# Performance work log

Measured on AMD Instinct MI355X. Metric: run time of the kernel, lower is better.

The kernel has to match this reference:

```python
import jax, jax.numpy as jnp
import numpy as np

B, T, C, H, W = 4, 5, 512, 32, 32   # bt = B*T = 20
G = 32                              # GroupNorm groups
EPS = 1e-6


def group_norm(x, gamma, beta):
    # x: [N, C, H, W]; normalize per (group-channels, H, W)
    n, c, h, w = x.shape
    xg = x.reshape(n, G, c // G, h * w)
    mu = jnp.mean(xg, axis=(2, 3), keepdims=True)
    var = jnp.mean((xg - mu) ** 2, axis=(2, 3), keepdims=True)
    xn = ((xg - mu) * jax.lax.rsqrt(var + EPS)).reshape(n, c, h, w)
    return xn * gamma[None, :, None, None] + beta[None, :, None, None]


def conv1x1(x, w, b):
    # 1x1 conv == channel matmul. x: [N,C,H,W], w: [O,C], b: [O]
    return jnp.einsum('nchw,oc->nohw', x, w) + b[None, :, None, None]


def setup_inputs() -> dict:
    key = jax.random.key(0)
    ks = jax.random.split(key, 9)
    inp = {'x': jax.random.normal(ks[0], (B * T, C, H, W), jnp.float32)}
    for i, nm in enumerate(['wq', 'wk', 'wv', 'wo', 'wqt', 'wkt', 'wvt', 'wot']):
        inp[nm] = jax.random.normal(ks[i + 1], (C, C), jnp.float32) * 0.02
        inp['b' + nm[1:]] = jnp.zeros((C,), jnp.float32)
    inp['gamma_s'] = jnp.ones((C,), jnp.float32)
    inp['beta_s'] = jnp.zeros((C,), jnp.float32)
    inp['gamma_t'] = jnp.ones((C,), jnp.float32)
    inp['beta_t'] = jnp.zeros((C,), jnp.float32)
    return inp


def reference(x, wq, bq, wk, bk, wv, bv, wo, bo,
              wqt, bqt, wkt, bkt, wvt, bvt, wot, bot,
              gamma_s, beta_s, gamma_t, beta_t):
    scale = float(C) ** -0.5

    # ---- spatial attention (AttnBlock.forward) ----
    hn = group_norm(x, gamma_s, beta_s)
    q = conv1x1(hn, wq, bq).reshape(B * T, C, H * W)
    k = conv1x1(hn, wk, bk).reshape(B * T, C, H * W)
    v = conv1x1(hn, wv, bv).reshape(B * T, C, H * W)
    # scores [bt, hw_q, hw_k], softmax over keys
    att = jax.nn.softmax(jnp.einsum('bcq,bck->bqk', q, k) * scale, axis=2)
    hsp = jnp.einsum('bck,bqk->bcq', v, att).reshape(B * T, C, H, W)
    spatio = x + conv1x1(hsp, wo, bo)

    # ---- temporal attention across t=5 frames per pixel ----
    hn = group_norm(spatio, gamma_t, beta_t)
    q5 = conv1x1(hn, wqt, bqt).reshape(B, T, C, H, W)
    k5 = conv1x1(hn, wkt, bkt).reshape(B, T, C, H, W)
    v5 = conv1x1(hn, wvt, bvt).reshape(B, T, C, H, W)
    # per-pixel [t, t] attention, softmax over key-frame axis s
    att_t = jax.nn.softmax(jnp.einsum('btchw,bschw->bhwts', q5, k5) * scale, axis=-1)
    htp = jnp.einsum('bhwts,bschw->btchw', att_t, v5).reshape(B * T, C, H, W)

    # NOTE: residual is the ORIGINAL x (faithful to the source), not spatio
    return x + conv1x1(htp, wot, bot)
```

## Files before the change

kernel.cpp:

```cpp
#include <hip/hip_runtime.h>
#include <hip/hip_bf16.h>
#include <stdint.h>

typedef unsigned short u16;
typedef __attribute__((ext_vector_type(8))) short bf16x8;
typedef __attribute__((ext_vector_type(4))) float f32x4;

#define DI __device__ __forceinline__

DI float b2f(u16 u) { return __uint_as_float(((uint32_t)u) << 16); }
DI u16 f2b(float f) {
  uint32_t u = __float_as_uint(f);
  u += 0x7fff + ((u >> 16) & 1);
  return (u16)(u >> 16);
}

DI void gld_lds16(const u16* g, u16* l) {
  __builtin_amdgcn_global_load_lds((const __attribute__((address_space(1))) void*)g,
                                   (__attribute__((address_space(3))) void*)l,
                                   16, 0, 0);
}

__global__ __launch_bounds__(256)
void prep(const float* __restrict__ x, const float* __restrict__ gamma,
          const float* __restrict__ beta, u16* __restrict__ gnout,
          const float* __restrict__ w0, const float* __restrict__ w1,
          const float* __restrict__ w2, const float* __restrict__ w3,
          const float* __restrict__ w4, const float* __restrict__ w5,
          const float* __restrict__ w6, const float* __restrict__ w7,
          const float* __restrict__ b0, const float* __restrict__ b1,
          const float* __restrict__ b2, const float* __restrict__ b3,
          const float* __restrict__ b4, const float* __restrict__ b5,
          const float* __restrict__ b6, const float* __restrict__ b7,
          u16* __restrict__ dst, float* __restrict__ bdst)
{
  const int t = threadIdx.x;
  if (blockIdx.x < 640) {
    const int w = (blockIdx.x & 7) * 80 + (blockIdx.x >> 3);
    const int n = w >> 5, g = w & 31;
    const int C = 512, HW = 1024;
    const float* xg = x + ((long)n * C + g * 16) * HW;
    float s = 0.f, ss = 0.f;
    for (int ch = t; ch < 4096; ch += 256) {
      float4 u = *(const float4*)(xg + ch * 4);
      s += u.x + u.y + u.z + u.w;
      ss += u.x * u.x + u.y * u.y + u.z * u.z + u.w * u.w;
    }
#pragma unroll
    for (int off = 32; off > 0; off >>= 1) { s += __shfl_xor(s, off); ss += __shfl_xor(ss, off); }
    __shared__ float rs[4], rss[4];
    if ((t & 63) == 0) { rs[t >> 6] = s; rss[t >> 6] = ss; }
    __syncthreads();
    s  = rs[0] + rs[1] + rs[2] + rs[3];
    ss = rss[0] + rss[1] + rss[2] + rss[3];
    const float mu = s * (1.f / 16384.f);
    const float var = ss * (1.f / 16384.f) - mu * mu;
    const float rstd = rsqrtf(var + 1e-6f);
    float gm[16], bt[16];
#pragma unroll
    for (int i = 0; i < 16; ++i) {
      float ga = gamma[g * 16 + i];
      gm[i] = ga * rstd;
      bt[i] = beta[g * 16 + i] - mu * ga * rstd;
    }
    for (int p = t; p < 1024; p += 256) {
      alignas(16) u16 vals[16];
#pragma unroll
      for (int i = 0; i < 16; ++i)
        vals[i] = f2b(xg[(long)i * HW + p] * gm[i] + bt[i]);
      u16* dp = gnout + ((long)n * HW + p) * C + g * 16;
      *(uint4*)dp       = *(const uint4*)&vals[0];
      *(uint4*)(dp + 8) = *(const uint4*)&vals[8];
    }
    return;
  }
  const int sb = blockIdx.x - 640;
  if (sb >= 1034) {
    bdst[8192 + (sb - 1034) * 256 + t] = 0.f;
    return;
  }
  if (sb >= 1032) {
    const int a = (sb - 1032) * 256 + t;
    float acc = 0.f;
    for (int c = 0; c < 512; ++c) acc += w3[a * 512 + c] * b2[c];
    bdst[4096 + a] = acc;
    return;
  }
  if (sb >= 1024) {
    const float* bs8[8] = {b0, b1, b2, b3, b4, b5, b6, b7};
    const int a = sb - 1024;
    bdst[a * 512 + t] = bs8[a][t];
    bdst[a * 512 + t + 256] = bs8[a][t + 256];
    return;
  }
  const float* srcs[8] = {w0, w1, w2, w3, w4, w5, w6, w7};
  const int mat = sb >> 7;
  const int i = (((sb & 127) << 8) + t) * 8;
  const float* s = srcs[mat];
  float4 a = *(const float4*)(s + i);
  float4 b = *(const float4*)(s + i + 4);
  alignas(16) u16 v[8] = {f2b(a.x), f2b(a.y), f2b(a.z), f2b(a.w),
                          f2b(b.x), f2b(b.y), f2b(b.z), f2b(b.w)};
  *(uint4*)(dst + (long)mat * 262144 + i) = *(const uint4*)v;
  if (mat == 2) {
    const int row = i >> 9, col = i & 511;
#pragma unroll
    for (int j = 0; j < 8; ++j) dst[8 * 262144 + (col + j) * 512 + row] = v[j];
  }
}

template<int OUTF32, int BIASMODE, int RESID, int SMEXP, int COLSCALE>
__global__ __launch_bounds__(256)
void gemm_bt(const u16* __restrict__ A, long sA, long lda,
             const u16* __restrict__ B, long sB, long ldb,
             void* __restrict__ C, long sC,
             const float* __restrict__ bias,
             const float* __restrict__ resid, long sR,
             int N, int K, float alpha, float* __restrict__ stats)
{
  __shared__ u16 lA[2 * 128 * 32];
  __shared__ u16 lB[2 * 128 * 32];
  const int t = threadIdx.x;
  const int lane = t & 63;
  const int wid = t >> 6;

  const uint32_t nx = gridDim.x, ny = gridDim.y;
  const uint32_t tpz = nx * ny;
  const uint32_t nblk = tpz * gridDim.z;
  const uint32_t g = ((uint32_t)blockIdx.z * ny + blockIdx.y) * nx + blockIdx.x;
  const uint32_t idx = (g & 7u) * (nblk >> 3) + (g >> 3);
  const uint32_t bz_ = idx / tpz;
  const uint32_t r   = idx - bz_ * tpz;
  const int m0 = (int)(r / nx) * 128, n0 = (int)(r % nx) * 128;
  const long bz = bz_;

  const u16* Ab = A + bz * sA;
  const u16* Bb = B + bz * sB;

  const int row = t >> 2;
  const int kc  = (((t & 3) ^ ((t >> 3) & 3)) << 3);

  f32x4 acc[4][4];
#pragma unroll
  for (int i = 0; i < 4; ++i)
#pragma unroll
    for (int j = 0; j < 4; ++j) acc[i][j] = (f32x4){0.f, 0.f, 0.f, 0.f};

  const int ml = lane & 15, qd = lane >> 4;
  const int koff = ((qd ^ ((ml >> 1) & 3)) << 3);
  const int wm = (wid >> 1) * 64, wn = (wid & 1) * 64;

  auto stage = [&](int bsel, int k0) {
    const u16* Ap = Ab + (long)(m0 + row) * lda + (k0 + kc);
    const u16* Bp = Bb + (long)(n0 + row) * ldb + (k0 + kc);
    u16* la = lA + bsel * 4096 + wid * 512;
    u16* lb = lB + bsel * 4096 + wid * 512;
    gld_lds16(Ap, la);
    gld_lds16(Ap + 64 * lda, la + 2048);
    gld_lds16(Bp, lb);
    gld_lds16(Bp + 64 * ldb, lb + 2048);
  };

  const int niter = K >> 5;
  stage(0, 0);
  for (int i = 0; i < niter; ++i) {
    __syncthreads();
    if (i + 1 < niter) stage((i + 1) & 1, (i + 1) << 5);
    const u16* la = lA + (i & 1) * 4096;
    const u16* lb = lB + (i & 1) * 4096;
    bf16x8 af[4], bfr[4];
#pragma unroll
    for (int x = 0; x < 4; ++x)
      af[x] = *(const bf16x8*)&la[(wm + x * 16 + ml) * 32 + koff];
#pragma unroll
    for (int y = 0; y < 4; ++y)
      bfr[y] = *(const bf16x8*)&lb[(wn + y * 16 + ml) * 32 + koff];
#pragma unroll
    for (int x = 0; x < 4; ++x)
#pragma unroll
      for (int y = 0; y < 4; ++y)
        acc[x][y] = __builtin_amdgcn_mfma_f32_16x16x32_bf16(af[x], bfr[y], acc[x][y], 0, 0, 0);
  }

  float inv[4];
  if (COLSCALE) {
#pragma unroll
    for (int j = 0; j < 4; ++j)
      inv[j] = 1.f / stats[bz * 1024 + n0 + wn + j * 16 + ml];
  }
  if (SMEXP) {
    float rs[16];
#pragma unroll
    for (int s = 0; s < 16; ++s) rs[s] = 0.f;
#pragma unroll
    for (int i = 0; i < 4; ++i)
#pragma unroll
      for (int j = 0; j < 4; ++j)
#pragma unroll
        for (int r2 = 0; r2 < 4; ++r2) {
          float e = __expf(acc[i][j][r2] * alpha);
          acc[i][j][r2] = e;
          rs[i * 4 + r2] += e;
        }
#pragma unroll
    for (int m = 1; m < 16; m <<= 1)
#pragma unroll
      for (int s = 0; s < 16; ++s) rs[s] += __shfl_xor(rs[s], m);
    if (ml == 0) {
#pragma unroll
      for (int i = 0; i < 4; ++i)
#pragma unroll
        for (int r2 = 0; r2 < 4; ++r2)
          atomicAdd(&stats[bz * 1024 + m0 + wm + i * 16 + qd * 4 + r2], rs[i * 4 + r2]);
    }
  }

  const long cb = bz * sC;
#pragma unroll
  for (int i = 0; i < 4; ++i) {
#pragma unroll
    for (int j = 0; j < 4; ++j) {
#pragma unroll
      for (int r2 = 0; r2 < 4; ++r2) {
        int rr = m0 + wm + i * 16 + qd * 4 + r2;
        int cc = n0 + wn + j * 16 + ml;
        float v = acc[i][j][r2];
        if (!SMEXP) v *= alpha;
        if (COLSCALE) v *= inv[j];
        if (BIASMODE == 1) v += bias[rr];
        if (BIASMODE == 2) v += bias[cc];
        long ix = (long)rr * N + cc;
        if (RESID) v += resid[bz * sR + ix];
        if (OUTF32) ((float*)C)[cb + ix] = v;
        else        ((u16*)C)[cb + ix] = f2b(v);
      }
    }
  }
}

template<int OUTF32, int BIASMODE, int RESID>
__global__ __launch_bounds__(512, 2)
void gemm256(const u16* __restrict__ A, long sA, long lda,
             const u16* __restrict__ B, long sB, long ldb,
             void* __restrict__ C, long sC,
             const float* __restrict__ bias,
             const float* __restrict__ resid, long sR,
             int N, int K, float alpha)
{
  __shared__ u16 lA[4 * 8192];
  __shared__ u16 lB[4 * 8192];
  const int t = threadIdx.x;
  const int lane = t & 63, wid = t >> 6;
  const int wr = wid >> 2, wc = wid & 3;
  const int ml = lane & 15, qd = lane >> 4;

  const int nx = gridDim.x;
  const int bid = blockIdx.y * nx + blockIdx.x;
  const int nper = (nx * gridDim.y) >> 3;
  const int nid = (bid & 7) * nper + (bid >> 3);
  const int m0 = (nid / nx) * 256, n0 = (nid % nx) * 256;

  const long bz = blockIdx.z;
  const u16* Ab = A + bz * sA;
  const u16* Bb = B + bz * sB;

  const int sw = ((lane & 3) ^ ((lane >> 3) & 3)) << 3;
  const int srow = wid * 32 + (lane >> 2);
  const u16* ApS = Ab + (long)(m0 + srow) * lda + sw;
  const u16* BpS = Bb + (long)(n0 + srow) * ldb + sw;
  u16* lwA = lA + wid * 1024;
  u16* lwB = lB + wid * 1024;

  f32x4 acc[8][4];
#pragma unroll
  for (int i = 0; i < 8; ++i)
#pragma unroll
    for (int j = 0; j < 4; ++j) acc[i][j] = (f32x4){0.f, 0.f, 0.f, 0.f};

  const int NT = K >> 5;

  auto stageA = [&](int tk) {
    const int bo = (tk & 3) << 13;
    const u16* p = ApS + ((long)tk << 5);
    gld_lds16(p,              lwA + bo);
    gld_lds16(p + (lda << 4), lwA + bo + 512);
  };
  auto stageB = [&](int tk) {
    const int bo = (tk & 3) << 13;
    const u16* p = BpS + ((long)tk << 5);
    gld_lds16(p,              lwB + bo);
    gld_lds16(p + (ldb << 4), lwB + bo + 512);
  };

  const int koff = (qd ^ ((ml >> 1) & 3)) << 3;
  const int rAo = (wr * 128 + ml) * 32 + koff;
  const int rBo = (wc * 64 + ml) * 32 + koff;

  stageA(0); stageB(0); stageA(1); stageB(1); stageA(2); stageB(2);
  asm volatile("s_waitcnt vmcnt(8)" ::: "memory");
  __builtin_amdgcn_s_barrier();
  __builtin_amdgcn_sched_barrier(0);

  for (int tk = 0; tk < NT; ++tk) {
    const int bo = (tk & 3) << 13;
    const u16* pa = lA + bo + rAo;
    const u16* pb = lB + bo + rBo;
    bf16x8 bfr[4], af[4];

#pragma unroll
    for (int n = 0; n < 4; ++n) bfr[n] = *(const bf16x8*)(pb + n * 512);
#pragma unroll
    for (int m = 0; m < 4; ++m) af[m] = *(const bf16x8*)(pa + m * 512);
    if (tk + 3 < NT) stageA(tk + 3);
    __builtin_amdgcn_sched_barrier(0);
    __builtin_amdgcn_s_barrier();
    asm volatile("s_waitcnt lgkmcnt(0)" ::: "memory");
    __builtin_amdgcn_sched_barrier(0);
    __builtin_amdgcn_s_setprio(1);
#pragma unroll
    for (int m = 0; m < 4; ++m)
#pragma unroll
      for (int n = 0; n < 4; ++n)
        acc[m][n] = __builtin_amdgcn_mfma_f32_16x16x32_bf16(af[m], bfr[n], acc[m][n], 0, 0, 0);
    __builtin_amdgcn_s_setprio(0);
    __builtin_amdgcn_sched_barrier(0);
    __builtin_amdgcn_s_barrier();
    __builtin_amdgcn_sched_barrier(0);

#pragma unroll
    for (int m = 0; m < 4; ++m) af[m] = *(const bf16x8*)(pa + (m + 4) * 512);
    if (tk + 3 < NT) stageB(tk + 3);
    __builtin_amdgcn_sched_barrier(0);
    __builtin_amdgcn_s_barrier();
    asm volatile("s_waitcnt lgkmcnt(0)" ::: "memory");
    __builtin_amdgcn_sched_barrier(0);
    __builtin_amdgcn_s_setprio(1);
#pragma unroll
    for (int m = 0; m < 4; ++m)
#pragma unroll
      for (int n = 0; n < 4; ++n)
        acc[m + 4][n] = __builtin_amdgcn_mfma_f32_16x16x32_bf16(af[m], bfr[n], acc[m + 4][n], 0, 0, 0);
    __builtin_amdgcn_s_setprio(0);
    __builtin_amdgcn_sched_barrier(0);

    if (tk < NT - 1) {
      const int rem = NT - 2 - tk;
      if (rem >= 2)      asm volatile("s_waitcnt vmcnt(8)" ::: "memory");
      else if (rem == 1) asm volatile("s_waitcnt vmcnt(4)" ::: "memory");
      else               asm volatile("s_waitcnt vmcnt(0)" ::: "memory");
      __builtin_amdgcn_s_barrier();
      __builtin_amdgcn_sched_barrier(0);
    }
  }

  const long cb = bz * sC;
#pragma unroll
  for (int mt = 0; mt < 8; ++mt) {
#pragma unroll
    for (int nt = 0; nt < 4; ++nt) {
#pragma unroll
      for (int r = 0; r < 4; ++r) {
        int rr = m0 + wr * 128 + mt * 16 + qd * 4 + r;
        int cc = n0 + wc * 64 + nt * 16 + ml;
        float v = acc[mt][nt][r] * alpha;
        if (BIASMODE == 1) v += bias[rr];
        if (BIASMODE == 2) v += bias[cc];
        long idx = (long)rr * N + cc;
        if (RESID) v += resid[bz * sR + idx];
        if (OUTF32) ((float*)C)[cb + idx] = v;
        else        ((u16*)C)[cb + idx] = f2b(v);
      }
    }
  }
}

__global__ __launch_bounds__(256)
void groupnorm_resid(const u16* __restrict__ h, const float* __restrict__ x,
                     const float* __restrict__ gamma,
                     const float* __restrict__ beta, u16* __restrict__ out)
{
  const int C = 512, HW = 1024;
  const int w = (blockIdx.x & 7) * 80 + (blockIdx.x >> 3);
  const int n = w >> 5, g = w & 31;
  const long base = ((long)n * C + g * 16) * HW;
  const float* xg = x + base;
  const u16*  hg = h + base;
  const int t = threadIdx.x;
  float s = 0.f, ss = 0.f;
  for (int ch = t; ch < 4096; ch += 256) {
    float4 u = *(const float4*)(xg + ch * 4);
    uint2 hv = *(const uint2*)(hg + ch * 4);
    float h0 = __uint_as_float(hv.x << 16);
    float h1 = __uint_as_float(hv.x & 0xffff0000u);
    float h2 = __uint_as_float(hv.y << 16);
    float h3 = __uint_as_float(hv.y & 0xffff0000u);
    float v0 = u.x + h0, v1 = u.y + h1, v2 = u.z + h2, v3 = u.w + h3;
    s += v0 + v1 + v2 + v3;
    ss += v0 * v0 + v1 * v1 + v2 * v2 + v3 * v3;
  }
#pragma unroll
  for (int off = 32; off > 0; off >>= 1) { s += __shfl_xor(s, off); ss += __shfl_xor(ss, off); }
  __shared__ float rs[4], rss[4];
  if ((t & 63) == 0) { rs[t >> 6] = s; rss[t >> 6] = ss; }
  __syncthreads();
  s  = rs[0] + rs[1] + rs[2] + rs[3];
  ss = rss[0] + rss[1] + rss[2] + rss[3];
  const float mu = s * (1.f / 16384.f);
  const float var = ss * (1.f / 16384.f) - mu * mu;
  const float rstd = rsqrtf(var + 1e-6f);
  float gm[16], bt[16];
#pragma unroll
  for (int i = 0; i < 16; ++i) {
    float ga = gamma[g * 16 + i];
    gm[i] = ga * rstd;
    bt[i] = beta[g * 16 + i] - mu * ga * rstd;
  }
  for (int p = t; p < 1024; p += 256) {
    alignas(16) u16 vals[16];
#pragma unroll
    for (int i = 0; i < 16; ++i)
      vals[i] = f2b((xg[(long)i * HW + p] + b2f(hg[(long)i * HW + p])) * gm[i] + bt[i]);
    u16* dst = out + ((long)n * HW + p) * C + g * 16;
    *(uint4*)dst       = *(const uint4*)&vals[0];
    *(uint4*)(dst + 8) = *(const uint4*)&vals[8];
  }
}

__global__ __launch_bounds__(256)
void temporal_attn(const u16* __restrict__ qkv, u16* __restrict__ htp)
{
  const int t = threadIdx.x;
  const int wv = t >> 6, lane = t & 63;
  const int pix = blockIdx.x * 4 + wv;
  const int b = pix >> 10, p = pix & 1023;
  const long fs = 1024l * 1536;
  const long rowbase = ((long)b * 5 * 1024 + p) * 1536 + lane * 8;

  float qf[5][8], kf[5][8];
#pragma unroll
  for (int f = 0; f < 5; ++f) {
    bf16x8 qv = *(const bf16x8*)(qkv + rowbase + f * fs);
    bf16x8 kv = *(const bf16x8*)(qkv + rowbase + f * fs + 512);
#pragma unroll
    for (int u = 0; u < 8; ++u) { qf[f][u] = b2f((u16)qv[u]); kf[f][u] = b2f((u16)kv[u]); }
  }
  float sc[25];
#pragma unroll
  for (int i = 0; i < 5; ++i)
#pragma unroll
    for (int j = 0; j < 5; ++j) {
      float a = 0.f;
#pragma unroll
      for (int u = 0; u < 8; ++u) a += qf[i][u] * kf[j][u];
      sc[i * 5 + j] = a;
    }
#pragma unroll
  for (int m = 1; m < 64; m <<= 1)
#pragma unroll
    for (int s = 0; s < 25; ++s) sc[s] += __shfl_xor(sc[s], m);

  const float scale = 0.04419417382415922f;
  float att[5][5];
#pragma unroll
  for (int i = 0; i < 5; ++i) {
    float m = sc[i * 5];
#pragma unroll
    for (int j = 1; j < 5; ++j) m = fmaxf(m, sc[i * 5 + j]);
    float ssum = 0.f;
#pragma unroll
    for (int j = 0; j < 5; ++j) { att[i][j] = __expf((sc[i * 5 + j] - m) * scale); ssum += att[i][j]; }
    float inv = 1.f / ssum;
#pragma unroll
    for (int j = 0; j < 5; ++j) att[i][j] *= inv;
  }

  float of[5][8];
#pragma unroll
  for (int i = 0; i < 5; ++i)
#pragma unroll
    for (int u = 0; u < 8; ++u) of[i][u] = 0.f;
#pragma unroll
  for (int s = 0; s < 5; ++s) {
    bf16x8 vvv = *(const bf16x8*)(qkv + rowbase + s * fs + 1024);
#pragma unroll
    for (int u = 0; u < 8; ++u) {
      float vf = b2f((u16)vvv[u]);
#pragma unroll
      for (int i = 0; i < 5; ++i) of[i][u] += att[i][s] * vf;
    }
  }
  const long obase = ((long)b * 5 * 1024 + p) * 512 + lane * 8;
#pragma unroll
  for (int i = 0; i < 5; ++i) {
    alignas(16) u16 ob[8];
#pragma unroll
    for (int u = 0; u < 8; ++u) ob[u] = f2b(of[i][u]);
    *(uint4*)(htp + obase + i * 1024 * 512) = *(const uint4*)ob;
  }
}

extern "C" void kernel_launch(void* const* d_in, const int* in_sizes, int n_in,
                              void* d_out, int out_size, void* d_ws, size_t ws_size,
                              hipStream_t stream)
{
  const float* x   = (const float*)d_in[0];
  const float* wq  = (const float*)d_in[1];
  const float* bq  = (const float*)d_in[2];
  const float* wk  = (const float*)d_in[3];
  const float* bk  = (const float*)d_in[4];
  const float* wv  = (const float*)d_in[5];
  const float* bv  = (const float*)d_in[6];
  const float* wo  = (const float*)d_in[7];
  const float* bo  = (const float*)d_in[8];
  const float* wqt = (const float*)d_in[9];
  const float* bqt = (const float*)d_in[10];
  const float* wkt = (const float*)d_in[11];
  const float* bkt = (const float*)d_in[12];
  const float* wvt = (const float*)d_in[13];
  const float* bvt = (const float*)d_in[14];
  const float* wot = (const float*)d_in[15];
  const float* bot = (const float*)d_in[16];
  const float* gs  = (const float*)d_in[17];
  const float* bs  = (const float*)d_in[18];
  const float* gt  = (const float*)d_in[19];
  const float* btt = (const float*)d_in[20];

  const long U = 20l * 1024 * 512;
  u16* W0 = (u16*)d_ws;
  u16* W1 = W0 + U;
  u16* W3 = W0 + 3 * U;
  u16* W4 = W0 + 4 * U;
  u16* W6 = W0 + 6 * U;
  u16* W7 = W0 + 7 * U;
  u16* Wt = W0 + 8 * U;
  u16* wvT_b = Wt + 8 * 262144;
  u16* Wovs  = Wt + 9 * 262144;
  float* Bf = (float*)(Wt + 10 * 262144);
  float* Stats = Bf + 8192;
  u16* wo_b  = Wt + 3 * 262144;
  u16* wqt_b = Wt + 4 * 262144;
  u16* wot_b = Wt + 7 * 262144;

  const long S  = 524288;
  const long S2 = 1048576;
  const float scale = 0.04419417382415922f;
  dim3 blk(256);
  dim3 blk5(512);

  prep<<<1754, blk, 0, stream>>>(x, gs, bs, W0,
                                 wq, wk, wv, wo, wqt, wkt, wvt, wot,
                                 bq, bk, bv, bo, bqt, bkt, bvt, bot, Wt, Bf);

  gemm_bt<0, 0, 0, 0, 0><<<dim3(4, 4, 1), blk, 0, stream>>>(
      wo_b, 0, 512, wvT_b, 0, 512, Wovs, 0, nullptr, nullptr, 0, 512, 512, 1.f, nullptr);

  gemm_bt<0, 2, 0, 0, 0><<<dim3(8, 160, 1), blk, 0, stream>>>(
      W0, 0, 512, Wt, 0, 512, W1, 0, Bf, nullptr, 0, 1024, 512, 1.f, nullptr);
  gemm_bt<0, 1, 0, 0, 0><<<dim3(8, 4, 20), blk, 0, stream>>>(
      Wovs, 0, 512, W0, S, 512, W3, S, Bf + 4096, nullptr, 0, 1024, 512, 1.f, nullptr);
  gemm_bt<0, 0, 0, 1, 0><<<dim3(8, 8, 20), blk, 0, stream>>>(
      W1, S2, 1024, W1 + 512, S2, 1024, W4, S2, nullptr, nullptr, 0, 1024, 512, scale, Stats);
  gemm_bt<0, 1, 0, 0, 1><<<dim3(8, 4, 20), blk, 0, stream>>>(
      W3, S, 1024, W4, S2, 1024, W6, S, Bf + 1536, nullptr, 0, 1024, 1024, 1.f, Stats);
  groupnorm_resid<<<640, blk, 0, stream>>>(W6, x, gt, btt, W7);
  gemm256<0, 2, 0><<<dim3(6, 80, 1), blk5, 0, stream>>>(
      W7, 0, 512, wqt_b, 0, 512, W1, 0, Bf + 2048, nullptr, 0, 1536, 512, 1.f);
  temporal_attn<<<1024, blk, 0, stream>>>(W1, W0);
  gemm_bt<1, 1, 1, 0, 0><<<dim3(8, 4, 20), blk, 0, stream>>>(
      wot_b, 0, 512, W0, S, 512, (float*)d_out, S, Bf + 3584, x, S, 1024, 512, 1.f, nullptr);
}
```

Baseline: 401.7 us.

## Fold temporal V projection into output projection weights

Computes Wot·Wvt as a combined matrix, using the same trick already applied to the spatial path. The temporal attention therefore reads the normalized input directly as V, and the QKV GEMM shrinks from 1536 to 1024 output columns. The folded bias Wot·bvt + bot is computed in prep, and the custom 256-tile gemm256 kernel is dropped in favor of gemm_bt. This removes one third of the temporal projection FLOPs and the V write/read, at the cost of an extra small 512x512 weight GEMM and losing the larger-tile kernel.

```diff
diff --git a/kernel.cpp b/kernel.cpp
--- a/kernel.cpp
+++ b/kernel.cpp
@@ -75,8 +75,15 @@
     return;
   }
   const int sb = blockIdx.x - 640;
+  if (sb >= 1036) {
+    bdst[8192 + (sb - 1036) * 256 + t] = 0.f;
+    return;
+  }
   if (sb >= 1034) {
-    bdst[8192 + (sb - 1034) * 256 + t] = 0.f;
+    const int a = (sb - 1034) * 256 + t;
+    float acc = 0.f;
+    for (int c = 0; c < 512; ++c) acc += w7[a * 512 + c] * b6[c];
+    bdst[4608 + a] = acc + b7[a];
     return;
   }
   if (sb >= 1032) {
@@ -102,10 +109,11 @@
   alignas(16) u16 v[8] = {f2b(a.x), f2b(a.y), f2b(a.z), f2b(a.w),
                           f2b(b.x), f2b(b.y), f2b(b.z), f2b(b.w)};
   *(uint4*)(dst + (long)mat * 262144 + i) = *(const uint4*)v;
-  if (mat == 2) {
+  if (mat == 2 || mat == 6) {
+    const int slot = (mat == 2) ? 8 : 10;
     const int row = i >> 9, col = i & 511;
 #pragma unroll
-    for (int j = 0; j < 8; ++j) dst[8 * 262144 + (col + j) * 512 + row] = v[j];
+    for (int j = 0; j < 8; ++j) dst[(long)slot * 262144 + (col + j) * 512 + row] = v[j];
   }
 }
 
@@ -233,142 +241,6 @@
         if (RESID) v += resid[bz * sR + ix];
         if (OUTF32) ((float*)C)[cb + ix] = v;
         else        ((u16*)C)[cb + ix] = f2b(v);
-      }
-    }
-  }
-}
-
-template<int OUTF32, int BIASMODE, int RESID>
-__global__ __launch_bounds__(512, 2)
-void gemm256(const u16* __restrict__ A, long sA, long lda,
-             const u16* __restrict__ B, long sB, long ldb,
-             void* __restrict__ C, long sC,
-             const float* __restrict__ bias,
-             const float* __restrict__ resid, long sR,
-             int N, int K, float alpha)
-{
-  __shared__ u16 lA[4 * 8192];
-  __shared__ u16 lB[4 * 8192];
-  const int t = threadIdx.x;
-  const int lane = t & 63, wid = t >> 6;
-  const int wr = wid >> 2, wc = wid & 3;
-  const int ml = lane & 15, qd = lane >> 4;
-
-  const int nx = gridDim.x;
-  const int bid = blockIdx.y * nx + blockIdx.x;
-  const int nper = (nx * gridDim.y) >> 3;
-  const int nid = (bid & 7) * nper + (bid >> 3);
-  const int m0 = (nid / nx) * 256, n0 = (nid % nx) * 256;
-
-  const long bz = blockIdx.z;
-  const u16* Ab = A + bz * sA;
-  const u16* Bb = B + bz * sB;
-
-  const int sw = ((lane & 3) ^ ((lane >> 3) & 3)) << 3;
-  const int srow = wid * 32 + (lane >> 2);
-  const u16* ApS = Ab + (long)(m0 + srow) * lda + sw;
-  const u16* BpS = Bb + (long)(n0 + srow) * ldb + sw;
-  u16* lwA = lA + wid * 1024;
-  u16* lwB = lB + wid * 1024;
-
-  f32x4 acc[8][4];
-#pragma unroll
-  for (int i = 0; i < 8; ++i)
-#pragma unroll
-    for (int j = 0; j < 4; ++j) acc[i][j] = (f32x4){0.f, 0.f, 0.f, 0.f};
-
-  const int NT = K >> 5;
-
-  auto stageA = [&](int tk) {
-    const int bo = (tk & 3) << 13;
-    const u16* p = ApS + ((long)tk << 5);
-    gld_lds16(p,              lwA + bo);
-    gld_lds16(p + (lda << 4), lwA + bo + 512);
-  };
-  auto stageB = [&](int tk) {
-    const int bo = (tk & 3) << 13;
-    const u16* p = BpS + ((long)tk << 5);
-    gld_lds16(p,              lwB + bo);
-    gld_lds16(p + (ldb << 4), lwB + bo + 512);
-  };
-
-  const int koff = (qd ^ ((ml >> 1) & 3)) << 3;
-  const int rAo = (wr * 128 + ml) * 32 + koff;
-  const int rBo = (wc * 64 + ml) * 32 + koff;
-
-  stageA(0); stageB(0); stageA(1); stageB(1); stageA(2); stageB(2);
-  asm volatile("s_waitcnt vmcnt(8)" ::: "memory");
-  __builtin_amdgcn_s_barrier();
-  __builtin_amdgcn_sched_barrier(0);
-
-  for (int tk = 0; tk < NT; ++tk) {
-    const int bo = (tk & 3) << 13;
-    const u16* pa = lA + bo + rAo;
-    const u16* pb = lB + bo + rBo;
-    bf16x8 bfr[4], af[4];
-
-#pragma unroll
-    for (int n = 0; n < 4; ++n) bfr[n] = *(const bf16x8*)(pb + n * 512);
-#pragma unroll
-    for (int m = 0; m < 4; ++m) af[m] = *(const bf16x8*)(pa + m * 512);
-    if (tk + 3 < NT) stageA(tk + 3);
-    __builtin_amdgcn_sched_barrier(0);
-    __builtin_amdgcn_s_barrier();
-    asm volatile("s_waitcnt lgkmcnt(0)" ::: "memory");
-    __builtin_amdgcn_sched_barrier(0);
-    __builtin_amdgcn_s_setprio(1);
-#pragma unroll
-    for (int m = 0; m < 4; ++m)
-#pragma unroll
-      for (int n = 0; n < 4; ++n)
-        acc[m][n] = __builtin_amdgcn_mfma_f32_16x16x32_bf16(af[m], bfr[n], acc[m][n], 0, 0, 0);
-    __builtin_amdgcn_s_setprio(0);
-    __builtin_amdgcn_sched_barrier(0);
-    __builtin_amdgcn_s_barrier();
-    __builtin_amdgcn_sched_barrier(0);
-
-#pragma unroll
-    for (int m = 0; m < 4; ++m) af[m] = *(const bf16x8*)(pa + (m + 4) * 512);
-    if (tk + 3 < NT) stageB(tk + 3);
-    __builtin_amdgcn_sched_barrier(0);
-    __builtin_amdgcn_s_barrier();
-    asm volatile("s_waitcnt lgkmcnt(0)" ::: "memory");
-    __builtin_amdgcn_sched_barrier(0);
-    __builtin_amdgcn_s_setprio(1);
-#pragma unroll
-    for (int m = 0; m < 4; ++m)
-#pragma unroll
-      for (int n = 0; n < 4; ++n)
-        acc[m + 4][n] = __builtin_amdgcn_mfma_f32_16x16x32_bf16(af[m], bfr[n], acc[m + 4][n], 0, 0, 0);
-    __builtin_amdgcn_s_setprio(0);
-    __builtin_amdgcn_sched_barrier(0);
-
-    if (tk < NT - 1) {
-      const int rem = NT - 2 - tk;
-      if (rem >= 2)      asm volatile("s_waitcnt vmcnt(8)" ::: "memory");
-      else if (rem == 1) asm volatile("s_waitcnt vmcnt(4)" ::: "memory");
-      else               asm volatile("s_waitcnt vmcnt(0)" ::: "memory");
-      __builtin_amdgcn_s_barrier();
-      __builtin_amdgcn_sched_barrier(0);
-    }
-  }
-
-  const long cb = bz * sC;
-#pragma unroll
-  for (int mt = 0; mt < 8; ++mt) {
-#pragma unroll
-    for (int nt = 0; nt < 4; ++nt) {
-#pragma unroll
-      for (int r = 0; r < 4; ++r) {
-        int rr = m0 + wr * 128 + mt * 16 + qd * 4 + r;
-        int cc = n0 + wc * 64 + nt * 16 + ml;
-        float v = acc[mt][nt][r] * alpha;
-        if (BIASMODE == 1) v += bias[rr];
-        if (BIASMODE == 2) v += bias[cc];
-        long idx = (long)rr * N + cc;
-        if (RESID) v += resid[bz * sR + idx];
-        if (OUTF32) ((float*)C)[cb + idx] = v;
-        else        ((u16*)C)[cb + idx] = f2b(v);
       }
     }
   }
@@ -427,20 +299,23 @@
 }
 
 __global__ __launch_bounds__(256)
-void temporal_attn(const u16* __restrict__ qkv, u16* __restrict__ htp)
+void temporal_attn(const u16* __restrict__ qk, const u16* __restrict__ hn,
+                   u16* __restrict__ htp)
 {
   const int t = threadIdx.x;
   const int wv = t >> 6, lane = t & 63;
   const int pix = blockIdx.x * 4 + wv;
   const int b = pix >> 10, p = pix & 1023;
-  const long fs = 1024l * 1536;
-  const long rowbase = ((long)b * 5 * 1024 + p) * 1536 + lane * 8;
+  const long fsq = 1024l * 1024;
+  const long rowq = ((long)b * 5 * 1024 + p) * 1024 + lane * 8;
+  const long fsh = 1024l * 512;
+  const long rowh = ((long)b * 5 * 1024 + p) * 512 + lane * 8;
 
   float qf[5][8], kf[5][8];
 #pragma unroll
   for (int f = 0; f < 5; ++f) {
-    bf16x8 qv = *(const bf16x8*)(qkv + rowbase + f * fs);
-    bf16x8 kv = *(const bf16x8*)(qkv + rowbase + f * fs + 512);
+    bf16x8 qv = *(const bf16x8*)(qk + rowq + f * fsq);
+    bf16x8 kv = *(const bf16x8*)(qk + rowq + f * fsq + 512);
 #pragma unroll
     for (int u = 0; u < 8; ++u) { qf[f][u] = b2f((u16)qv[u]); kf[f][u] = b2f((u16)kv[u]); }
   }
@@ -481,7 +356,7 @@
     for (int u = 0; u < 8; ++u) of[i][u] = 0.f;
 #pragma unroll
   for (int s = 0; s < 5; ++s) {
-    bf16x8 vvv = *(const bf16x8*)(qkv + rowbase + s * fs + 1024);
+    bf16x8 vvv = *(const bf16x8*)(hn + rowh + s * fsh);
 #pragma unroll
     for (int u = 0; u < 8; ++u) {
       float vf = b2f((u16)vvv[u]);
@@ -489,13 +364,12 @@
       for (int i = 0; i < 5; ++i) of[i][u] += att[i][s] * vf;
     }
   }
-  const long obase = ((long)b * 5 * 1024 + p) * 512 + lane * 8;
 #pragma unroll
   for (int i = 0; i < 5; ++i) {
     alignas(16) u16 ob[8];
 #pragma unroll
     for (int u = 0; u < 8; ++u) ob[u] = f2b(of[i][u]);
-    *(uint4*)(htp + obase + i * 1024 * 512) = *(const uint4*)ob;
+    *(uint4*)(htp + rowh + i * fsh) = *(const uint4*)ob;
   }
 }
 
@@ -533,39 +407,39 @@
   u16* W6 = W0 + 6 * U;
   u16* W7 = W0 + 7 * U;
   u16* Wt = W0 + 8 * U;
-  u16* wvT_b = Wt + 8 * 262144;
-  u16* Wovs  = Wt + 9 * 262144;
-  float* Bf = (float*)(Wt + 10 * 262144);
+  u16* wvT_b  = Wt + 8 * 262144;
+  u16* Wovs   = Wt + 9 * 262144;
+  u16* Wovt_b = Wt + 11 * 262144;
+  float* Bf = (float*)(Wt + 12 * 262144);
   float* Stats = Bf + 8192;
   u16* wo_b  = Wt + 3 * 262144;
   u16* wqt_b = Wt + 4 * 262144;
-  u16* wot_b = Wt + 7 * 262144;
 
   const long S  = 524288;
   const long S2 = 1048576;
   const float scale = 0.04419417382415922f;
   dim3 blk(256);
-  dim3 blk5(512);
-
-  prep<<<1754, blk, 0, stream>>>(x, gs, bs, W0,
+
+  prep<<<1756, blk, 0, stream>>>(x, gs, bs, W0,
                                  wq, wk, wv, wo, wqt, wkt, wvt, wot,
                                  bq, bk, bv, bo, bqt, bkt, bvt, bot, Wt, Bf);
 
-  gemm_bt<0, 0, 0, 0, 0><<<dim3(4, 4, 1), blk, 0, stream>>>(
-      wo_b, 0, 512, wvT_b, 0, 512, Wovs, 0, nullptr, nullptr, 0, 512, 512, 1.f, nullptr);
+  gemm_bt<0, 0, 0, 0, 0><<<dim3(4, 4, 2), blk, 0, stream>>>(
+      wo_b, 4 * 262144, 512, wvT_b, 2 * 262144, 512, Wovs, 2 * 262144,
+      nullptr, nullptr, 0, 512, 512, 1.f, nullptr);
 
   gemm_bt<0, 2, 0, 0, 0><<<dim3(8, 160, 1), blk, 0, stream>>>(
       W0, 0, 512, Wt, 0, 512, W1, 0, Bf, nullptr, 0, 1024, 512, 1.f, nullptr);
   gemm_bt<0, 1, 0, 0, 0><<<dim3(8, 4, 20), blk, 0, stream>>>(
-      Wovs, 0, 512, W0, S, 512, W3, S, Bf + 4096, nullptr, 0, 1024, 512, 1.f, nullptr);
+      Wovs, 0, 512, W0, S, 512, W3, S, Bf + 4096, nullptr, 0, 1024, 512, 1.f, Stats);
   gemm_bt<0, 0, 0, 1, 0><<<dim3(8, 8, 20), blk, 0, stream>>>(
       W1, S2, 1024, W1 + 512, S2, 1024, W4, S2, nullptr, nullptr, 0, 1024, 512, scale, Stats);
   gemm_bt<0, 1, 0, 0, 1><<<dim3(8, 4, 20), blk, 0, stream>>>(
       W3, S, 1024, W4, S2, 1024, W6, S, Bf + 1536, nullptr, 0, 1024, 1024, 1.f, Stats);
   groupnorm_resid<<<640, blk, 0, stream>>>(W6, x, gt, btt, W7);
-  gemm256<0, 2, 0><<<dim3(6, 80, 1), blk5, 0, stream>>>(
-      W7, 0, 512, wqt_b, 0, 512, W1, 0, Bf + 2048, nullptr, 0, 1536, 512, 1.f);
-  temporal_attn<<<1024, blk, 0, stream>>>(W1, W0);
+  gemm_bt<0, 2, 0, 0, 0><<<dim3(8, 160, 1), blk, 0, stream>>>(
+      W7, 0, 512, wqt_b, 0, 512, W1, 0, Bf + 2048, nullptr, 0, 1024, 512, 1.f, nullptr);
+  temporal_attn<<<1024, blk, 0, stream>>>(W1, W7, W0);
   gemm_bt<1, 1, 1, 0, 0><<<dim3(8, 4, 20), blk, 0, stream>>>(
-      wot_b, 0, 512, W0, S, 512, (float*)d_out, S, Bf + 3584, x, S, 1024, 512, 1.f, nullptr);
-}
+      Wovt_b, 0, 512, W0, S, 512, (float*)d_out, S, Bf + 4608, x, S, 1024, 512, 1.f, nullptr);
+}
```

Measured after the change: 391.8 us. 2.5% less time.
